# Performance work log

Hardware: AMD Instinct MI355X
Metric: run time of the kernel (lower is better)

## Reference

```python
import jax, jax.numpy as jnp
import numpy as np

N_NODES = 100000
N_EDGES = 3200000
N_FEAT = 512
N_CLASS = 40
HIDDEN = 16


def _agnn(x, src, dst, beta, num_nodes):
    # PyG AGNNConv: cosine-similarity attention, softmax over incoming edges.
    norm = jnp.linalg.norm(x, axis=1, keepdims=True)
    x_norm = x / jnp.maximum(norm, 1e-12)
    # per-edge logits: beta * <x_norm_dst, x_norm_src>
    alpha = beta * jnp.sum(x_norm[dst] * x_norm[src], axis=1)  # [E]
    # segment softmax over destination nodes
    m = jax.ops.segment_max(alpha, dst, num_segments=num_nodes)  # [N]
    e = jnp.exp(alpha - m[dst])
    s = jax.ops.segment_sum(e, dst, num_segments=num_nodes)  # [N]
    w = e / jnp.maximum(s[dst], 1e-16)  # [E]
    # weighted aggregation of source features to destination
    return jax.ops.segment_sum(x[src] * w[:, None], dst, num_segments=num_nodes)


def setup_inputs() -> dict:
    key = jax.random.key(0)
    ks = jax.random.split(key, 7)
    x = jax.random.normal(ks[0], (N_NODES, N_FEAT), dtype=jnp.float32)
    edge_index = jax.random.randint(ks[1], (2, N_EDGES), 0, N_NODES, dtype=jnp.int32)
    lin1_w = jax.random.normal(ks[2], (HIDDEN, N_FEAT), dtype=jnp.float32) * (1.0 / np.sqrt(N_FEAT))
    lin1_b = jax.random.normal(ks[3], (HIDDEN,), dtype=jnp.float32) * 0.01
    beta2 = jnp.ones((1,), dtype=jnp.float32)
    lin2_w = jax.random.normal(ks[4], (N_CLASS, HIDDEN), dtype=jnp.float32) * (1.0 / np.sqrt(HIDDEN))
    lin2_b = jax.random.normal(ks[5], (N_CLASS,), dtype=jnp.float32) * 0.01
    return {"x": x, "edge_index": edge_index, "lin1_w": lin1_w, "lin1_b": lin1_b,
            "beta2": beta2, "lin2_w": lin2_w, "lin2_b": lin2_b}


def reference(x, edge_index, lin1_w, lin1_b, beta2, lin2_w, lin2_b):
    src, dst = edge_index[0], edge_index[1]
    n = x.shape[0]
    # eval mode: dropout is identity
    h = jax.nn.relu(x @ lin1_w.T + lin1_b)          # [N, 16]
    h = _agnn(h, src, dst, jnp.float32(1.0), n)     # prop1: beta fixed at 1
    h = _agnn(h, src, dst, beta2[0], n)             # prop2: learnable beta
    logits = h @ lin2_w.T + lin2_b                  # [N, C]
    return jax.nn.log_softmax(logits, axis=1)
```

## Files before the change

### kernel.cpp

```cpp
#include <hip/hip_runtime.h>

#define N_NODES 100000
#define N_EDGES 3200000
#define N_FEAT  512
#define HID     16
#define N_CLASS 40

#define BSHIFT  9
#define BMASK   ((1 << BSHIFT) - 1)
#define NB      196
#define CAP     18432
#define EPB     4096
#define EC_CAP  3072

#define BIN_BLOCKS  ((N_EDGES + EPB - 1) / EPB)
#define NT_TILES    (N_NODES / 16)
#define LIN1_BLOCKS ((NT_TILES + 3) / 4)

typedef __attribute__((ext_vector_type(8))) short bf16x8;
typedef __attribute__((ext_vector_type(4))) float f32x4;

__device__ inline short2 split_bf(float v) {
    const unsigned u = __float_as_uint(v);
    const short hi = (short)(u >> 16);
    const float hf = __uint_as_float(u & 0xFFFF0000u);
    const short lo = (short)(__float_as_uint(v - hf) >> 16);
    return make_short2(hi, lo);
}
__device__ inline unsigned short f2bf_rtn(float v) {
    unsigned u = __float_as_uint(v);
    u += 0x7FFFu + ((u >> 16) & 1u);
    return (unsigned short)(u >> 16);
}
__device__ inline float bf2f(unsigned short u) {
    return __uint_as_float(((unsigned)u) << 16);
}

struct BinSmem {
    int hist[NB]; int lofs[NB]; int base[NB]; int rk[NB];
    int buf[256]; int stage[EPB]; unsigned short sbkt[EPB];
};
struct Lin1Smem { short bfH[16 * 64 * 8]; short bfL[16 * 64 * 8]; };

__device__ void bin_body(char* smemraw,
                         const int* __restrict__ src,
                         const int* __restrict__ dst,
                         int* __restrict__ cursor,
                         int* __restrict__ binned) {
    BinSmem& sm = *(BinSmem*)smemraw;
    const int t = threadIdx.x;
    for (int i = t; i < NB; i += 256) { sm.hist[i] = 0; sm.rk[i] = 0; }
    __syncthreads();

    const int e0 = blockIdx.x * EPB;
    int bk[EPB / 256];
    int vv[EPB / 256];
#pragma unroll
    for (int k = 0; k < EPB / 256; k++) {
        const int e = e0 + k * 256 + t;
        if (e < N_EDGES) {
            const int d = dst[e], s = src[e];
            bk[k] = d >> BSHIFT;
            vv[k] = (s << BSHIFT) | (d & BMASK);
            atomicAdd(&sm.hist[bk[k]], 1);
        } else bk[k] = -1;
    }
    __syncthreads();

    {
        const int v = (t < NB) ? sm.hist[t] : 0;
        sm.buf[t] = v; __syncthreads();
        for (int o = 1; o < 256; o <<= 1) {
            const int a = (t >= o) ? sm.buf[t - o] : 0;
            __syncthreads();
            sm.buf[t] += a;
            __syncthreads();
        }
        if (t < NB) sm.lofs[t] = sm.buf[t] - v;
    }
    if (t < NB && sm.hist[t] > 0)
        sm.base[t] = t * CAP + atomicAdd(&cursor[t], sm.hist[t]);

#pragma unroll
    for (int k = 0; k < EPB / 256; k++) {
        if (bk[k] >= 0) {
            const int r = atomicAdd(&sm.rk[bk[k]], 1);
            const int slot = sm.lofs[bk[k]] + r;
            sm.stage[slot] = vv[k];
            sm.sbkt[slot] = (unsigned short)bk[k];
        }
    }
    __syncthreads();

    const int nloc = min(EPB, N_EDGES - e0);
    for (int s2 = t; s2 < nloc; s2 += 256) {
        const int b = sm.sbkt[s2];
        binned[sm.base[b] + (s2 - sm.lofs[b])] = sm.stage[s2];
    }
}

__device__ void lin1_body(char* smemraw, int lblk,
                          const float* __restrict__ x,
                          const float* __restrict__ w1,
                          const float* __restrict__ b1,
                          unsigned short* __restrict__ xnb,
                          float* __restrict__ normv) {
    Lin1Smem& sm = *(Lin1Smem*)smemraw;
    const int t = threadIdx.x;
    for (int f = t; f < 16 * 64; f += 256) {
        const int kt  = f >> 6;
        const int ln  = f & 63;
        const int col = ln & 15;
        const int k0  = kt * 32 + (ln >> 4) * 8;
        const float4 v0 = *(const float4*)(w1 + col * N_FEAT + k0);
        const float4 v1 = *(const float4*)(w1 + col * N_FEAT + k0 + 4);
        bf16x8 hh, ll;
        short2 r;
        r = split_bf(v0.x); hh[0] = r.x; ll[0] = r.y;
        r = split_bf(v0.y); hh[1] = r.x; ll[1] = r.y;
        r = split_bf(v0.z); hh[2] = r.x; ll[2] = r.y;
        r = split_bf(v0.w); hh[3] = r.x; ll[3] = r.y;
        r = split_bf(v1.x); hh[4] = r.x; ll[4] = r.y;
        r = split_bf(v1.y); hh[5] = r.x; ll[5] = r.y;
        r = split_bf(v1.z); hh[6] = r.x; ll[6] = r.y;
        r = split_bf(v1.w); hh[7] = r.x; ll[7] = r.y;
        ((bf16x8*)sm.bfH)[f] = hh;
        ((bf16x8*)sm.bfL)[f] = ll;
    }
    __syncthreads();

    const int wv   = t >> 6;
    const int l    = t & 63;
    const int tile = lblk * 4 + wv;
    if (tile >= NT_TILES) return;

    const int r0 = tile * 16;
    const float* xp = x + (size_t)(r0 + (l & 15)) * N_FEAT + ((l >> 4) * 8);

    f32x4 acc = {0.f, 0.f, 0.f, 0.f};
    float4 c0 = *(const float4*)(xp);
    float4 c1 = *(const float4*)(xp + 4);
#pragma unroll
    for (int kt = 0; kt < 16; ++kt) {
        float4 n0, n1;
        if (kt < 15) {
            n0 = *(const float4*)(xp + (kt + 1) * 32);
            n1 = *(const float4*)(xp + (kt + 1) * 32 + 4);
        }
        bf16x8 ah, al;
        short2 r;
        r = split_bf(c0.x); ah[0] = r.x; al[0] = r.y;
        r = split_bf(c0.y); ah[1] = r.x; al[1] = r.y;
        r = split_bf(c0.z); ah[2] = r.x; al[2] = r.y;
        r = split_bf(c0.w); ah[3] = r.x; al[3] = r.y;
        r = split_bf(c1.x); ah[4] = r.x; al[4] = r.y;
        r = split_bf(c1.y); ah[5] = r.x; al[5] = r.y;
        r = split_bf(c1.z); ah[6] = r.x; al[6] = r.y;
        r = split_bf(c1.w); ah[7] = r.x; al[7] = r.y;
        const bf16x8 bh = ((const bf16x8*)sm.bfH)[kt * 64 + l];
        const bf16x8 bl = ((const bf16x8*)sm.bfL)[kt * 64 + l];
        acc = __builtin_amdgcn_mfma_f32_16x16x32_bf16(ah, bh, acc, 0, 0, 0);
        acc = __builtin_amdgcn_mfma_f32_16x16x32_bf16(al, bh, acc, 0, 0, 0);
        acc = __builtin_amdgcn_mfma_f32_16x16x32_bf16(ah, bl, acc, 0, 0, 0);
        c0 = n0; c1 = n1;
    }

    const float bias = b1[l & 15];
#pragma unroll
    for (int r = 0; r < 4; ++r) {
        const float v = fmaxf(acc[r] + bias, 0.f);
        float ss = v * v;
        ss += __shfl_xor(ss, 1); ss += __shfl_xor(ss, 2);
        ss += __shfl_xor(ss, 4); ss += __shfl_xor(ss, 8);
        const float nrm = sqrtf(ss);
        const float rn  = 1.f / fmaxf(nrm, 1e-12f);
        const int row = r0 + (l >> 4) * 4 + r;
        xnb[(size_t)row * HID + (l & 15)] = f2bf_rtn(v * rn);
        if ((l & 15) == 0) normv[row] = nrm;
    }
}

__global__ __launch_bounds__(256) void k_bin_lin1(const int* __restrict__ src,
                                                  const int* __restrict__ dst,
                                                  int* __restrict__ cursor,
                                                  int* __restrict__ binned,
                                                  const float* __restrict__ x,
                                                  const float* __restrict__ w1,
                                                  const float* __restrict__ b1,
                                                  unsigned short* __restrict__ xnb,
                                                  float* __restrict__ normv) {
    __shared__ __align__(16) char smem[sizeof(Lin1Smem) > sizeof(BinSmem)
                                       ? sizeof(Lin1Smem) : sizeof(BinSmem)];
    if (blockIdx.x < BIN_BLOCKS)
        bin_body(smem, src, dst, cursor, binned);
    else
        lin1_body(smem, blockIdx.x - BIN_BLOCKS, x, w1, b1, xnb, normv);
}

__global__ __launch_bounds__(512) void k_csr(const int* __restrict__ cursor,
                                             int* __restrict__ binned,
                                             int* __restrict__ row_start,
                                             unsigned short* __restrict__ row_cnt) {
    __shared__ int cnts[512];
    __shared__ int cur[512];
    __shared__ int buf[512];
    __shared__ int lcsr[CAP];

    const int t = threadIdx.x;
    const int b = blockIdx.x;
    const int s0 = b * CAP;
    const int n = cursor[b];

    cnts[t] = 0;
    __syncthreads();
    for (int i = t; i < n; i += 512)
        atomicAdd(&cnts[binned[s0 + i] & BMASK], 1);
    __syncthreads();

    {
        const int v = cnts[t];
        buf[t] = v; __syncthreads();
        for (int o = 1; o < 512; o <<= 1) {
            const int a = (t >= o) ? buf[t - o] : 0;
            __syncthreads();
            buf[t] += a;
            __syncthreads();
        }
        cur[t] = buf[t] - v;
        const int node = (b << BSHIFT) + t;
        if (node < N_NODES) {
            row_start[node] = s0 + cur[t];
            row_cnt[node]   = (unsigned short)v;
        }
    }
    __syncthreads();

    for (int i = t; i < n; i += 512) {
        const int v = binned[s0 + i];
        const int p = atomicAdd(&cur[v & BMASK], 1);
        lcsr[p] = v >> BSHIFT;
    }
    __syncthreads();

    for (int i = t; i < n; i += 512) binned[s0 + i] = lcsr[i];
}

template <int LAST>
__global__ __launch_bounds__(256) void k_agnn(const int* __restrict__ row_start,
                                              const unsigned short* __restrict__ row_cnt,
                                              const int* __restrict__ csr_src,
                                              const unsigned short* __restrict__ xnb,
                                              const float* __restrict__ normv,
                                              const float* __restrict__ betap,
                                              const float* __restrict__ w2,
                                              const float* __restrict__ b2,
                                              float* __restrict__ out,
                                              unsigned short* __restrict__ outb,
                                              float* __restrict__ out_norm) {
    __shared__ int ldsCsr[EC_CAP];
    __shared__ float w2s[HID][N_CLASS + 1];
    __shared__ float b2s[N_CLASS];
    __shared__ int sRs0, sNE;

    const int t256 = threadIdx.x;
    const int ls   = t256 & 3;
    const int node = blockIdx.x * 64 + (t256 >> 2);
    const bool alive = node < N_NODES;

    if (LAST) {
        for (int i = t256; i < N_CLASS * HID; i += 256)
            w2s[i % HID][i / HID] = w2[i];
        if (t256 < N_CLASS) b2s[t256] = b2[t256];
    }

    const int rs  = alive ? row_start[node] : 0;
    const int cnt = alive ? (int)row_cnt[node] : 0;

    if (t256 == 0) {
        const int base = blockIdx.x * 64;
        const int last = min(base + 64, N_NODES) - 1;
        const int r0 = row_start[base];
        sRs0 = r0;
        sNE  = row_start[last] + (int)row_cnt[last] - r0;
    }
    __syncthreads();
    const int rs0 = sRs0;
    const int nStage = min(sNE, EC_CAP);
    for (int i = t256; i < nStage; i += 256)
        ldsCsr[i] = csr_src[rs0 + i];
    __syncthreads();

    const float beta  = betap ? betap[0] : 1.0f;
    const float shift = fabsf(beta);
    const int off = rs - rs0;

    const int nodeSafe = alive ? node : 0;
    const bf16x8* xd = (const bf16x8*)(xnb + (size_t)nodeSafe * HID);
    const bf16x8 dlo = xd[0], dhi = xd[1];
    float dd[16];
#pragma unroll
    for (int i = 0; i < 8; i++) {
        dd[i]     = bf2f((unsigned short)dlo[i]);
        dd[i + 8] = bf2f((unsigned short)dhi[i]);
    }

    int mcnt = (cnt + 3) >> 2;
#pragma unroll
    for (int m = 1; m < 64; m <<= 1) mcnt = max(mcnt, __shfl_xor(mcnt, m));

    float acc[16];
#pragma unroll
    for (int i = 0; i < 16; i++) acc[i] = 0.f;
    float swl = 0.f;

    bool ok = (ls < cnt);
    int sidx = 0;
    if (ok) { const int p = off + ls; sidx = (p < nStage) ? ldsCsr[p] : csr_src[rs + ls]; }
    const bf16x8* xs0 = (const bf16x8*)(xnb + (size_t)sidx * HID);
    bf16x8 slo = xs0[0], shi = xs0[1];
    float nj = normv[sidx];

    for (int t = 0; t < mcnt; ++t) {
        const int e2 = 4 * (t + 1) + ls;
        const bool ok2 = (e2 < cnt);
        int sidx2 = 0;
        if (ok2) {
            const int p = off + e2;
            sidx2 = (p < nStage) ? ldsCsr[p] : csr_src[rs + e2];
        }
        const bf16x8* xs2 = (const bf16x8*)(xnb + (size_t)sidx2 * HID);
        const bf16x8 slo2 = xs2[0], shi2 = xs2[1];
        const float nj2 = normv[sidx2];

        float sr[16];
#pragma unroll
        for (int i = 0; i < 8; i++) {
            sr[i]     = bf2f((unsigned short)slo[i]);
            sr[i + 8] = bf2f((unsigned short)shi[i]);
        }
        float p0 = 0.f, p1 = 0.f, p2 = 0.f, p3 = 0.f;
#pragma unroll
        for (int i = 0; i < 4; i++) {
            p0 += sr[i]      * dd[i];
            p1 += sr[i + 4]  * dd[i + 4];
            p2 += sr[i + 8]  * dd[i + 8];
            p3 += sr[i + 12] * dd[i + 12];
        }
        const float dot = (p0 + p1) + (p2 + p3);
        const float w = ok ? __expf(beta * dot - shift) : 0.f;
        swl += w;
        const float wn = w * nj;
#pragma unroll
        for (int i = 0; i < 16; i++) acc[i] += wn * sr[i];

        slo = slo2; shi = shi2; nj = nj2; ok = ok2;
    }

#pragma unroll
    for (int m = 1; m < 4; m <<= 1) {
#pragma unroll
        for (int i = 0; i < 16; i++) acc[i] += __shfl_xor(acc[i], m);
        swl += __shfl_xor(swl, m);
    }

    const float inv = 1.f / fmaxf(swl, 1e-16f);
    float v[16];
#pragma unroll
    for (int i = 0; i < 16; i++) v[i] = acc[i] * inv;

    if (!LAST) {
        float ss = 0.f;
#pragma unroll
        for (int i = 0; i < 16; i++) ss += v[i] * v[i];
        const float nrm = sqrtf(ss);
        const float rn  = 1.f / fmaxf(nrm, 1e-12f);
        if (alive && ls == 0) {
            bf16x8 o0, o1;
#pragma unroll
            for (int i = 0; i < 8; i++) {
                o0[i] = (short)f2bf_rtn(v[i] * rn);
                o1[i] = (short)f2bf_rtn(v[i + 8] * rn);
            }
            bf16x8* orow = (bf16x8*)(outb + (size_t)node * HID);
            orow[0] = o0; orow[1] = o1;
            out_norm[node] = nrm;
        }
    } else {
        const int j0 = ls * 10;
        float lg[10];
#pragma unroll
        for (int j = 0; j < 10; j++) lg[j] = b2s[j0 + j];
#pragma unroll
        for (int k = 0; k < HID; k++) {
            const float vk = v[k];
#pragma unroll
            for (int j = 0; j < 10; j++) lg[j] += vk * w2s[k][j0 + j];
        }
        float m = -3.0e38f;
#pragma unroll
        for (int j = 0; j < 10; j++) m = fmaxf(m, lg[j]);
        m = fmaxf(m, __shfl_xor(m, 1)); m = fmaxf(m, __shfl_xor(m, 2));
        float s = 0.f;
#pragma unroll
        for (int j = 0; j < 10; j++) s += __expf(lg[j] - m);
        s += __shfl_xor(s, 1); s += __shfl_xor(s, 2);
        const float lse = m + __logf(s);
        if (alive) {
            float* orow = out + (size_t)node * N_CLASS + j0;
#pragma unroll
            for (int j = 0; j < 10; j++) orow[j] = lg[j] - lse;
        }
    }
}

extern "C" void kernel_launch(void* const* d_in, const int* in_sizes, int n_in,
                              void* d_out, int out_size, void* d_ws, size_t ws_size,
                              hipStream_t stream) {
    const float* x     = (const float*)d_in[0];
    const int*   ei    = (const int*)  d_in[1];
    const float* w1    = (const float*)d_in[2];
    const float* b1    = (const float*)d_in[3];
    const float* beta2 = (const float*)d_in[4];
    const float* w2    = (const float*)d_in[5];
    const float* b2    = (const float*)d_in[6];
    float* out = (float*)d_out;

    const int* srcp = ei;
    const int* dstp = ei + N_EDGES;

    unsigned short* xnb1 = (unsigned short*)d_ws;
    unsigned short* xnb2 = xnb1 + (size_t)N_NODES * HID;
    float* norm1 = (float*)(xnb2 + (size_t)N_NODES * HID);
    float* norm2 = norm1 + N_NODES;
    int* row_start = (int*)(norm2 + N_NODES);
    unsigned short* row_cnt = (unsigned short*)(row_start + N_NODES);
    int* cursor = (int*)(row_cnt + N_NODES + (N_NODES & 1));
    int* binned = cursor + NB + 2;

    const int agnnGrid = (N_NODES + 63) / 64;

    hipMemsetAsync(cursor, 0, NB * sizeof(int), stream);

    k_bin_lin1<<<BIN_BLOCKS + LIN1_BLOCKS, 256, 0, stream>>>(
        srcp, dstp, cursor, binned, x, w1, b1, xnb1, norm1);

    k_csr<<<NB, 512, 0, stream>>>(cursor, binned, row_start, row_cnt);

    k_agnn<0><<<agnnGrid, 256, 0, stream>>>(row_start, row_cnt, binned, xnb1,
                                            norm1, nullptr, nullptr, nullptr,
                                            nullptr, xnb2, norm2);
    k_agnn<1><<<agnnGrid, 256, 0, stream>>>(row_start, row_cnt, binned, xnb2,
                                            norm2, beta2, w2, b2,
                                            out, nullptr, nullptr);
}
```

Measured before the change: 166.7 us.

## Sort nodes by in-degree within each bin to balance AGNN wavefront work

The CSR build kernel now counting-sorts each 512-node bin by in-degree (capped at 127) and writes a node permutation. Both AGNN kernels map threads to nodes through that permutation, so nodes with similar edge counts share a wavefront and the max-count loop bound idles fewer lanes. Because permuted nodes are no longer contiguous, the LDS staging of CSR source indices is removed and indices are read straight from global memory. This adds an extra indirection and scattered row_start and feature reads.

```diff
diff --git a/kernel.cpp b/kernel.cpp
--- a/kernel.cpp
+++ b/kernel.cpp
@@ -11,7 +11,6 @@
 #define NB      196
 #define CAP     18432
 #define EPB     4096
-#define EC_CAP  3072
 
 #define BIN_BLOCKS  ((N_EDGES + EPB - 1) / EPB)
 #define NT_TILES    (N_NODES / 16)
@@ -200,7 +199,8 @@
 __global__ __launch_bounds__(512) void k_csr(const int* __restrict__ cursor,
                                              int* __restrict__ binned,
                                              int* __restrict__ row_start,
-                                             unsigned short* __restrict__ row_cnt) {
+                                             unsigned short* __restrict__ row_cnt,
+                                             int* __restrict__ nodeperm) {
     __shared__ int cnts[512];
     __shared__ int cur[512];
     __shared__ int buf[512];
@@ -243,10 +243,38 @@
     __syncthreads();
 
     for (int i = t; i < n; i += 512) binned[s0 + i] = lcsr[i];
+
+    __syncthreads();
+    if (t < 128) buf[t] = 0;
+    __syncthreads();
+    const int nodeT = (b << BSHIFT) + t;
+    const bool aliveT = nodeT < N_NODES;
+    int myb = 0;
+    if (aliveT) {
+        myb = min(cnts[t], 127);
+        atomicAdd(&buf[myb], 1);
+    }
+    __syncthreads();
+    if (t < 128) cur[t] = buf[t];
+    __syncthreads();
+    for (int o = 1; o < 128; o <<= 1) {
+        int a = 0;
+        if (t < 128 && t >= o) a = cur[t - o];
+        __syncthreads();
+        if (t < 128) cur[t] += a;
+        __syncthreads();
+    }
+    if (t < 128) cur[t] -= buf[t];
+    __syncthreads();
+    if (aliveT) {
+        const int r = atomicAdd(&cur[myb], 1);
+        nodeperm[(b << BSHIFT) + r] = nodeT;
+    }
 }
 
 template <int LAST>
-__global__ __launch_bounds__(256) void k_agnn(const int* __restrict__ row_start,
+__global__ __launch_bounds__(256) void k_agnn(const int* __restrict__ nodeperm,
+                                              const int* __restrict__ row_start,
                                               const unsigned short* __restrict__ row_cnt,
                                               const int* __restrict__ csr_src,
                                               const unsigned short* __restrict__ xnb,
@@ -257,45 +285,29 @@
                                               float* __restrict__ out,
                                               unsigned short* __restrict__ outb,
                                               float* __restrict__ out_norm) {
-    __shared__ int ldsCsr[EC_CAP];
     __shared__ float w2s[HID][N_CLASS + 1];
     __shared__ float b2s[N_CLASS];
-    __shared__ int sRs0, sNE;
 
     const int t256 = threadIdx.x;
     const int ls   = t256 & 3;
-    const int node = blockIdx.x * 64 + (t256 >> 2);
-    const bool alive = node < N_NODES;
+    const int gid  = blockIdx.x * 64 + (t256 >> 2);
+    const bool alive = gid < N_NODES;
+    const int node = alive ? nodeperm[gid] : 0;
 
     if (LAST) {
         for (int i = t256; i < N_CLASS * HID; i += 256)
             w2s[i % HID][i / HID] = w2[i];
         if (t256 < N_CLASS) b2s[t256] = b2[t256];
+        __syncthreads();
     }
 
     const int rs  = alive ? row_start[node] : 0;
     const int cnt = alive ? (int)row_cnt[node] : 0;
 
-    if (t256 == 0) {
-        const int base = blockIdx.x * 64;
-        const int last = min(base + 64, N_NODES) - 1;
-        const int r0 = row_start[base];
-        sRs0 = r0;
-        sNE  = row_start[last] + (int)row_cnt[last] - r0;
-    }
-    __syncthreads();
-    const int rs0 = sRs0;
-    const int nStage = min(sNE, EC_CAP);
-    for (int i = t256; i < nStage; i += 256)
-        ldsCsr[i] = csr_src[rs0 + i];
-    __syncthreads();
-
     const float beta  = betap ? betap[0] : 1.0f;
     const float shift = fabsf(beta);
-    const int off = rs - rs0;
-
-    const int nodeSafe = alive ? node : 0;
-    const bf16x8* xd = (const bf16x8*)(xnb + (size_t)nodeSafe * HID);
+
+    const bf16x8* xd = (const bf16x8*)(xnb + (size_t)node * HID);
     const bf16x8 dlo = xd[0], dhi = xd[1];
     float dd[16];
 #pragma unroll
@@ -314,8 +326,7 @@
     float swl = 0.f;
 
     bool ok = (ls < cnt);
-    int sidx = 0;
-    if (ok) { const int p = off + ls; sidx = (p < nStage) ? ldsCsr[p] : csr_src[rs + ls]; }
+    int sidx = ok ? csr_src[rs + ls] : 0;
     const bf16x8* xs0 = (const bf16x8*)(xnb + (size_t)sidx * HID);
     bf16x8 slo = xs0[0], shi = xs0[1];
     float nj = normv[sidx];
@@ -323,11 +334,7 @@
     for (int t = 0; t < mcnt; ++t) {
         const int e2 = 4 * (t + 1) + ls;
         const bool ok2 = (e2 < cnt);
-        int sidx2 = 0;
-        if (ok2) {
-            const int p = off + e2;
-            sidx2 = (p < nStage) ? ldsCsr[p] : csr_src[rs + e2];
-        }
+        const int sidx2 = ok2 ? csr_src[rs + e2] : 0;
         const bf16x8* xs2 = (const bf16x8*)(xnb + (size_t)sidx2 * HID);
         const bf16x8 slo2 = xs2[0], shi2 = xs2[1];
         const float nj2 = normv[sidx2];
@@ -434,7 +441,8 @@
     float* norm2 = norm1 + N_NODES;
     int* row_start = (int*)(norm2 + N_NODES);
     unsigned short* row_cnt = (unsigned short*)(row_start + N_NODES);
-    int* cursor = (int*)(row_cnt + N_NODES + (N_NODES & 1));
+    int* nodeperm = (int*)(row_cnt + N_NODES + (N_NODES & 1));
+    int* cursor = nodeperm + N_NODES;
     int* binned = cursor + NB + 2;
 
     const int agnnGrid = (N_NODES + 63) / 64;
@@ -444,12 +452,12 @@
     k_bin_lin1<<<BIN_BLOCKS + LIN1_BLOCKS, 256, 0, stream>>>(
         srcp, dstp, cursor, binned, x, w1, b1, xnb1, norm1);
 
-    k_csr<<<NB, 512, 0, stream>>>(cursor, binned, row_start, row_cnt);
-
-    k_agnn<0><<<agnnGrid, 256, 0, stream>>>(row_start, row_cnt, binned, xnb1,
-                                            norm1, nullptr, nullptr, nullptr,
-                                            nullptr, xnb2, norm2);
-    k_agnn<1><<<agnnGrid, 256, 0, stream>>>(row_start, row_cnt, binned, xnb2,
-                                            norm2, beta2, w2, b2,
+    k_csr<<<NB, 512, 0, stream>>>(cursor, binned, row_start, row_cnt, nodeperm);
+
+    k_agnn<0><<<agnnGrid, 256, 0, stream>>>(nodeperm, row_start, row_cnt, binned,
+                                            xnb1, norm1, nullptr, nullptr,
+                                            nullptr, nullptr, xnb2, norm2);
+    k_agnn<1><<<agnnGrid, 256, 0, stream>>>(nodeperm, row_start, row_cnt, binned,
+                                            xnb2, norm2, beta2, w2, b2,
                                             out, nullptr, nullptr);
 }
```

After: 209.0 us. 1.25x slower.
